# Kernel optimization log

Measured on AMD Instinct MI355X. Metric: run time of the kernel, lower is better.

## Reference

```python
import jax, jax.numpy as jnp
import numpy as np

C = 10  # cluster gap window; repo-level global constant in the original code


def _per_neuron(v, label):
    """Faithful vectorized translation of the per-(batch,neuron) Python loops.

    v:     [T] membrane potential trace
    label: scalar int target cluster count
    Returns (loss_contribution, num_cluster).
    """
    T = v.shape[0]
    t = jnp.arange(T, dtype=jnp.int32)
    spk = v >= 0.0                                   # spike positions (v >= 0)
    # exclusive prefix counts of spikes: csp[i] = #spikes in v[:i]
    csp = jnp.concatenate([jnp.zeros(1, jnp.int32), jnp.cumsum(spk.astype(jnp.int32))])
    lo = jnp.clip(t - C, 0, T)
    # a spike starts a new cluster iff no spike in the preceding C steps
    cnt_prev = csp[t] - csp[lo]
    is_start = spk & (cnt_prev == 0)
    num_cluster = jnp.sum(is_start.astype(jnp.int32))
    vmax = jnp.max(v)

    # ---- excess branch (label > num_cluster) ----
    # mask[t] = 1 iff some spike lies in [t-C, t+C]  (union of [first-C, last+C] per cluster)
    hi = jnp.clip(t + C + 1, 0, T)
    mask = (csp[hi] - csp[lo]) > 0
    full0 = jnp.all(mask)
    NEG = jnp.asarray(-1e30, v.dtype)
    m0 = jnp.max(jnp.where(mask, NEG, v))            # max over unmasked times (iter 0)
    tm = jnp.argmax(v)                               # original uses global argmax of v
    win = (t >= tm - C // 2) & (t <= tm + C // 2)
    mask2 = mask | win                               # mask after first loop iteration (fixed thereafter)
    full2 = jnp.all(mask2)
    # if mask2 full, remaining iterations pick a spike value (random in original; spikes have v>=0,
    # we use the deterministic surrogate vmax which is always a spike value when spikes exist)
    m_rest = jnp.where(full2, vmax, jnp.max(jnp.where(mask2, NEG, v)))
    label_f = label.astype(v.dtype)
    ncf = num_cluster.astype(v.dtype)
    dE = jnp.maximum(label_f - ncf, 1.0)             # safe denominator (branch-gated below)
    mean_excess = (m0 + (dE - 1.0) * m_rest) / dE
    excess_loss = jnp.where(full0, vmax, -mean_excess)

    # ---- deficit branch (label < num_cluster) ----
    BIG = T + 2 * C + 2
    lt = jax.lax.cummax(jnp.where(spk, t, -BIG))                 # nearest spike <= t
    rt = jax.lax.cummin(jnp.where(spk, t, BIG)[::-1])[::-1]      # nearest spike >= t
    in_span = (rt - lt) <= C                                     # t inside [first,last] of a cluster
    cid = jnp.cumsum(is_start.astype(jnp.int32)) - 1             # cluster id at time t
    K = T // (C + 1) + 1                                         # max possible clusters
    seg = jnp.where(in_span, cid, K)
    rec = jax.ops.segment_max(v, seg, num_segments=K + 1)[:K]    # per-cluster span max
    POS = jnp.asarray(1e30, v.dtype)
    rec = jnp.where(jnp.arange(K) < num_cluster, rec, POS)
    rec = jnp.sort(rec)                                          # ascending, real clusters first
    dD = jnp.maximum(ncf - label_f, 1.0)
    deficit_loss = jnp.sum(jnp.where(jnp.arange(K) < (num_cluster - label), rec, 0.0)) / dD

    contrib = jnp.where(label > num_cluster, excess_loss,
                        jnp.where(label < num_cluster, deficit_loss, 0.0))
    return contrib, num_cluster


def setup_inputs() -> dict:
    key = jax.random.key(0)
    k1, k2, k3 = jax.random.split(key, 3)
    B, T, N = 256, 500, 128
    vmem = jax.random.normal(k1, (B, T, N), dtype=jnp.float32)
    vlastmem = jax.random.normal(k2, (B, T, N), dtype=jnp.float32)
    labels_t = jax.random.randint(k3, (B, N), 0, 5, dtype=jnp.int32)
    return {"vmem": vmem, "vlastmem": vlastmem, "labels_t": labels_t, "ratio": 1}


def reference(vmem, vlastmem, labels_t, ratio):
    # vlastmem and ratio are unused in the original forward; kept for signature fidelity.
    vv = jnp.transpose(vmem, (0, 2, 1))  # [B, N, T]
    contrib, nclus = jax.vmap(jax.vmap(_per_neuron))(vv, labels_t)
    loss = jnp.sum(contrib)
    spike_output = nclus.astype(jnp.float32)  # [B, N] cluster counts
    return loss, spike_output
```

## Files before the change

kernel.cpp:

```cpp
#include <hip/hip_runtime.h>

namespace {
constexpr int CC    = 10;
constexpr int TT    = 500;
constexpr int NN    = 128;
constexpr int G     = 10;
constexpr int LSEG  = TT / G;
constexpr int HALO  = CC;
constexpr int NSLOT = 10;
constexpr int MAXG  = TT / (CC + 1) + 1;
}

__global__ __launch_bounds__(128, 5)
void seg_scan_kernel(const float* __restrict__ vmem, float* __restrict__ ws) {
    const int s   = blockIdx.x;
    const int b   = blockIdx.y;
    const int tid = threadIdx.x;
    const int a   = s * LSEG;
    const float* __restrict__ col = vmem + (size_t)b * TT * NN + tid;

    __shared__ float stg[5 * NN];

    float b0[10], b1[10], b2[10], b3[10] = {};
    auto load = [&](float (&d)[10], int c) {
        #pragma unroll
        for (int j = 0; j < 10; ++j) {
            int t = a + (-HALO + 10 * c + j);
            t = t < 0 ? 0 : (t > TT - 1 ? TT - 1 : t);
            d[j] = col[(size_t)t * NN];
        }
    };

    int   ls = -(1 << 20), lcount = 0, hdne = 0, tmn = 0, hasu = 0;
    float ccm = -1e30f, rmax = -1e30f, hdm = -1e30f, vmx = -1e30f, m0 = -1e30f;
    const bool firstSeg = (s == 0), lastSeg = (s == G - 1);
    #pragma unroll
    for (int i = 0; i < 5; ++i) stg[i * NN + tid] = 0.0f;

    auto scan = [&](const float (&cur)[10], const float (&prev)[10], int c) {
        #pragma unroll
        for (int j = 0; j < 10; ++j) {
            const int ofs = -HALO + 10 * c + j;
            const int t   = a + ofs;
            float v = cur[j];
            if ((ofs < 0 && firstSeg) || (ofs >= LSEG && lastSeg)) v = -1.0f;
            const bool spike = v >= 0.0f;
            if (ofs >= 0 && ofs < LSEG) {
                const float rm2 = fmaxf(rmax, v);
                if (spike) {
                    if (t - ls > CC) {
                        if (lcount > 0) stg[(lcount - 1) * NN + tid] = ccm;
                        ccm = v; ++lcount;
                    } else if (lcount == 0) { hdne = 1; hdm = fmaxf(hdm, rm2); }
                    else ccm = fmaxf(ccm, rm2);
                    rmax = -1e30f;
                } else rmax = rm2;
                if (v > vmx) { vmx = v; tmn = t; }
            }
            if (spike) ls = t;
            if (ofs >= HALO) {
                const float vu = prev[j];
                if (ls < t - 2 * CC) { hasu = 1; if (vu > m0) m0 = vu; }
            }
        }
    };

    load(b0, 0); load(b1, 1);
    load(b2, 2); scan(b0, b3, 0);
    load(b3, 3); scan(b1, b0, 1);
    load(b0, 4); scan(b2, b1, 2);
    load(b1, 5); scan(b3, b2, 3);
    load(b2, 6); scan(b0, b3, 4);
    scan(b1, b0, 5);
    scan(b2, b1, 6);

    if (lcount > 0) stg[(lcount - 1) * NN + tid] = ccm;

    float* __restrict__ wsl = ws + (size_t)(b * G + s) * NSLOT * NN + tid;
    #pragma unroll
    for (int i = 0; i < 5; ++i) wsl[i * NN] = stg[i * NN + tid];
    const int packed = lcount | (hdne << 3) | (hasu << 4) | (tmn << 5);
    wsl[5 * NN] = __int_as_float(packed);
    wsl[6 * NN] = hdm;
    wsl[7 * NN] = rmax;
    wsl[8 * NN] = vmx;
    wsl[9 * NN] = m0;
}

__global__ __launch_bounds__(64)
void merge_kernel(const float* __restrict__ vmem, const float* __restrict__ ws,
                  const int* __restrict__ labels, float* __restrict__ out) {
    const int bb = blockIdx.x, lane = threadIdx.x;
    const int b = bb >> 1, n = ((bb & 1) << 6) | lane;
    __shared__ float gl[MAXG * 64];
    __shared__ float wb[512];

    const float* __restrict__ wsb = ws + (size_t)b * G * NSLOT * NN + n;
    float f[2][10];
    auto loadSeg = [&](int slot, int s2) {
        const float* p = wsb + (size_t)s2 * NSLOT * NN;
        #pragma unroll
        for (int i = 0; i < 10; ++i) f[slot][i] = p[i * NN];
    };
    loadSeg(0, 0);

    int g = 0, g_nc = 0, g_hasu = 0, g_tm = 0;
    bool open = false; float cur = -1e30f, ptg = -1e30f;
    float g_vmax = -1e30f, g_m0 = -1e30f;
    #pragma unroll
    for (int s2 = 0; s2 < G; ++s2) {
        if (s2 + 1 < G) loadSeg((s2 + 1) & 1, s2 + 1);
        const float (&d)[10] = f[s2 & 1];
        const int pk = __float_as_int(d[5]);
        const int k = pk & 7, hne = (pk >> 3) & 1;
        g_nc += k; g_hasu |= (pk >> 4) & 1;
        if (d[8] > g_vmax) { g_vmax = d[8]; g_tm = pk >> 5; }
        if (d[9] > g_m0) g_m0 = d[9];
        if (open) {
            if (hne) { cur = fmaxf(cur, fmaxf(ptg, d[6])); ptg = d[7]; }
            if (k > 0 || !hne) { gl[g * 64 + lane] = cur; ++g; open = false; }
        }
        if (k > 0) {
            #pragma unroll
            for (int i = 0; i < 4; ++i)
                if (i < k - 1) { gl[g * 64 + lane] = d[i]; ++g; }
            float last = d[4];
            if (k == 1) last = d[0];
            else if (k == 2) last = d[1];
            else if (k == 3) last = d[2];
            else if (k == 4) last = d[3];
            cur = last; open = true; ptg = d[7];
        }
    }
    if (open) { gl[g * 64 + lane] = cur; ++g; }

    const int label = labels[b * NN + n];

    const bool need2 = (label > g_nc) && g_hasu && (label - g_nc >= 2);
    float mrest = g_vmax;
    unsigned long long bal = __ballot(need2);
    const float* colbase = vmem + (size_t)b * TT * NN;
    while (bal) {
        const int fl = __ffsll((unsigned long long)bal) - 1;
        bal &= bal - 1;
        const int   nf    = ((bb & 1) << 6) | fl;
        const int   tmf   = __shfl(g_tm, fl);
        const float vmaxf = __shfl(g_vmax, fl);
        #pragma unroll
        for (int j = 0; j < 8; ++j) {
            const int t = lane * 8 + j;
            wb[t] = (t < TT) ? colbase[(size_t)t * NN + nf] : -1.0f;
        }
        __syncthreads();
        int ls2 = -1000, lh = 0; float lm = -1e30f;
        const int u0 = lane * 8;
        for (int t2 = u0 - 10; t2 < u0 + 18; ++t2) {
            const float v = (t2 >= 0 && t2 < 512) ? wb[t2] : -1.0f;
            if (v >= 0.0f) ls2 = t2;
            const int u = t2 - 10;
            if (u >= u0 && u < u0 + 8 && u < TT) {
                if (ls2 < u - 10 && (u < tmf - CC / 2 || u > tmf + CC / 2)) {
                    lh = 1; const float vu = wb[u]; if (vu > lm) lm = vu;
                }
            }
        }
        #pragma unroll
        for (int off = 32; off > 0; off >>= 1) {
            lm = fmaxf(lm, __shfl_down(lm, off));
            lh |= __shfl_down(lh, off);
        }
        const float res = __shfl(lh ? lm : vmaxf, 0);
        if (lane == fl) mrest = res;
        __syncthreads();
    }

    float contrib = 0.0f;
    if (label > g_nc) {
        if (!g_hasu) contrib = g_vmax;
        else {
            const float dE = (float)(label - g_nc);
            contrib = -((g_m0 + (dE - 1.0f) * mrest) / dE);
        }
    } else if (label < g_nc) {
        const int kk = g_nc - label;
        float ssum = 0.0f;
        for (int i = 0; i < kk; ++i) {
            float mn = 1e30f; int mj = 0;
            for (int jj = 0; jj < g_nc; ++jj) {
                const float x = gl[jj * 64 + lane];
                if (x < mn) { mn = x; mj = jj; }
            }
            ssum += mn; gl[mj * 64 + lane] = 1e30f;
        }
        contrib = ssum / (float)kk;
    }

    out[1 + b * NN + n] = (float)g_nc;

    float w = contrib;
    #pragma unroll
    for (int off = 32; off > 0; off >>= 1) w += __shfl_down(w, off);
    if (lane == 0) atomicAdd(out, w);
}

extern "C" void kernel_launch(void* const* d_in, const int* in_sizes, int n_in,
                              void* d_out, int out_size, void* d_ws, size_t ws_size,
                              hipStream_t stream) {
    const float* vmem   = (const float*)d_in[0];
    const int*   labels = (const int*)d_in[2];
    float*       out    = (float*)d_out;
    float*       ws     = (float*)d_ws;

    const int B = in_sizes[2] / NN;

    hipMemsetAsync(out, 0, sizeof(float), stream);
    hipLaunchKernelGGL(seg_scan_kernel, dim3(G, B), dim3(NN), 0, stream, vmem, ws);
    hipLaunchKernelGGL(merge_kernel, dim3(2 * B), dim3(64), 0, stream, vmem, ws, labels, out);
}
```

Measured before the change: 164.5 us.

## Load whole segment into registers and make the scan loop branchless

Replaces the rotating 4-buffer software-pipelined load/scan with a single upfront load of all 70 rows into registers. The per-row cluster scan becomes branch-free selects, and the current cluster max is written to shared memory on every step instead of only when a cluster closes. Unused slots are zeroed at write-out. Occupancy hint drops from 5 to 4 blocks per CU to make room for the extra registers. All loads are issued early to expose memory parallelism, at the cost of higher register pressure and more LDS stores.

```diff
diff --git a/kernel.cpp b/kernel.cpp
--- a/kernel.cpp
+++ b/kernel.cpp
@@ -7,11 +7,12 @@
 constexpr int G     = 10;
 constexpr int LSEG  = TT / G;
 constexpr int HALO  = CC;
+constexpr int ROWS  = LSEG + 2 * HALO;
 constexpr int NSLOT = 10;
 constexpr int MAXG  = TT / (CC + 1) + 1;
 }
 
-__global__ __launch_bounds__(128, 5)
+__global__ __launch_bounds__(128, 4)
 void seg_scan_kernel(const float* __restrict__ vmem, float* __restrict__ ws) {
     const int s   = blockIdx.x;
     const int b   = blockIdx.y;
@@ -21,64 +22,60 @@
 
     __shared__ float stg[5 * NN];
 
-    float b0[10], b1[10], b2[10], b3[10] = {};
-    auto load = [&](float (&d)[10], int c) {
-        #pragma unroll
-        for (int j = 0; j < 10; ++j) {
-            int t = a + (-HALO + 10 * c + j);
-            t = t < 0 ? 0 : (t > TT - 1 ? TT - 1 : t);
-            d[j] = col[(size_t)t * NN];
-        }
-    };
+    float v[ROWS];
+    #pragma unroll
+    for (int r = 0; r < ROWS; ++r) {
+        int t = a - HALO + r;
+        t = t < 0 ? 0 : (t > TT - 1 ? TT - 1 : t);
+        v[r] = col[(size_t)t * NN];
+    }
+    if (s == 0) {
+        #pragma unroll
+        for (int r = 0; r < HALO; ++r) v[r] = -1.0f;
+    }
+    if (s == G - 1) {
+        #pragma unroll
+        for (int r = LSEG + HALO; r < ROWS; ++r) v[r] = -1.0f;
+    }
 
     int   ls = -(1 << 20), lcount = 0, hdne = 0, tmn = 0, hasu = 0;
     float ccm = -1e30f, rmax = -1e30f, hdm = -1e30f, vmx = -1e30f, m0 = -1e30f;
-    const bool firstSeg = (s == 0), lastSeg = (s == G - 1);
-    #pragma unroll
-    for (int i = 0; i < 5; ++i) stg[i * NN + tid] = 0.0f;
-
-    auto scan = [&](const float (&cur)[10], const float (&prev)[10], int c) {
-        #pragma unroll
-        for (int j = 0; j < 10; ++j) {
-            const int ofs = -HALO + 10 * c + j;
-            const int t   = a + ofs;
-            float v = cur[j];
-            if ((ofs < 0 && firstSeg) || (ofs >= LSEG && lastSeg)) v = -1.0f;
-            const bool spike = v >= 0.0f;
-            if (ofs >= 0 && ofs < LSEG) {
-                const float rm2 = fmaxf(rmax, v);
-                if (spike) {
-                    if (t - ls > CC) {
-                        if (lcount > 0) stg[(lcount - 1) * NN + tid] = ccm;
-                        ccm = v; ++lcount;
-                    } else if (lcount == 0) { hdne = 1; hdm = fmaxf(hdm, rm2); }
-                    else ccm = fmaxf(ccm, rm2);
-                    rmax = -1e30f;
-                } else rmax = rm2;
-                if (v > vmx) { vmx = v; tmn = t; }
-            }
-            if (spike) ls = t;
-            if (ofs >= HALO) {
-                const float vu = prev[j];
-                if (ls < t - 2 * CC) { hasu = 1; if (vu > m0) m0 = vu; }
-            }
-        }
-    };
-
-    load(b0, 0); load(b1, 1);
-    load(b2, 2); scan(b0, b3, 0);
-    load(b3, 3); scan(b1, b0, 1);
-    load(b0, 4); scan(b2, b1, 2);
-    load(b1, 5); scan(b3, b2, 3);
-    load(b2, 6); scan(b0, b3, 4);
-    scan(b1, b0, 5);
-    scan(b2, b1, 6);
-
-    if (lcount > 0) stg[(lcount - 1) * NN + tid] = ccm;
+
+    #pragma unroll
+    for (int r = 0; r < ROWS; ++r) {
+        const int ofs = r - HALO;
+        const int t   = a + ofs;
+        const float x = v[r];
+        const bool spike = x >= 0.0f;
+        if (ofs >= 0 && ofs < LSEG) {
+            const float rm2     = fmaxf(rmax, x);
+            const bool  recent  = (t - ls <= CC);
+            const bool  isStart = spike && !recent;
+            const bool  contS   = spike && recent;
+            const bool  hd      = contS && (lcount == 0);
+            hdm  = hd ? fmaxf(hdm, rm2) : hdm;
+            hdne = hd ? 1 : hdne;
+            const float folded = fmaxf(ccm, rm2);
+            ccm  = isStart ? x : ((contS && lcount > 0) ? folded : ccm);
+            lcount += isStart ? 1 : 0;
+            rmax = spike ? -1e30f : rm2;
+            if (x > vmx) { vmx = x; tmn = t; }
+            const int idx = lcount > 0 ? lcount - 1 : 0;
+            stg[idx * NN + tid] = ccm;
+        }
+        if (spike) ls = t;
+        if (r >= 2 * HALO) {
+            const float vu = v[r - HALO];
+            const bool  um = ls < t - 2 * CC;
+            hasu = um ? 1 : hasu;
+            m0   = um ? fmaxf(m0, vu) : m0;
+        }
+    }
 
     float* __restrict__ wsl = ws + (size_t)(b * G + s) * NSLOT * NN + tid;
     #pragma unroll
-    for (int i = 0; i < 5; ++i) wsl[i * NN] = stg[i * NN + tid];
+    for (int i = 0; i < 5; ++i)
+        wsl[i * NN] = (i < lcount) ? stg[i * NN + tid] : 0.0f;
     const int packed = lcount | (hdne << 3) | (hasu << 4) | (tmn << 5);
     wsl[5 * NN] = __int_as_float(packed);
     wsl[6 * NN] = hdm;
```

After: 256.2 us. 55.7% more time.

## Pack more wavefronts per block and make segment scan branch-free

Applied to the files above, without the earlier changes.

The segment scan kernel now packs ten wavefronts into a 640-thread block, with each wave covering one segment-half and using its own shared staging area. The scan body is rewritten as predicated selects, and it writes the current cluster max to shared memory on every step instead of only at cluster boundaries. The merge kernel now runs four independent wavefronts per 256-thread block with per-wave shared buffers, and replaces __syncthreads with block fences because each wave only touches its own buffers. The aim is to cut block count and launch and scheduling overhead and to reduce divergence, at the cost of extra shared stores per step and lower occupancy from the larger blocks.

```diff
diff --git a/kernel.cpp b/kernel.cpp
--- a/kernel.cpp
+++ b/kernel.cpp
@@ -11,15 +11,20 @@
 constexpr int MAXG  = TT / (CC + 1) + 1;
 }
 
-__global__ __launch_bounds__(128, 5)
+__global__ __launch_bounds__(640, 5)
 void seg_scan_kernel(const float* __restrict__ vmem, float* __restrict__ ws) {
-    const int s   = blockIdx.x;
-    const int b   = blockIdx.y;
-    const int tid = threadIdx.x;
-    const int a   = s * LSEG;
-    const float* __restrict__ col = vmem + (size_t)b * TT * NN + tid;
-
-    __shared__ float stg[5 * NN];
+    const int z    = blockIdx.x;
+    const int b    = blockIdx.y;
+    const int tid  = threadIdx.x;
+    const int ww   = tid >> 6;
+    const int lane = tid & 63;
+    const int s    = z * 5 + (ww >> 1);
+    const int half = ww & 1;
+    const int a    = s * LSEG;
+    const float* __restrict__ col = vmem + (size_t)b * TT * NN + half * 64 + lane;
+
+    __shared__ float stg[10][5 * 64];
+    float* sw = stg[ww];
 
     float b0[10], b1[10], b2[10], b3[10] = {};
     auto load = [&](float (&d)[10], int c) {
@@ -34,33 +39,37 @@
     int   ls = -(1 << 20), lcount = 0, hdne = 0, tmn = 0, hasu = 0;
     float ccm = -1e30f, rmax = -1e30f, hdm = -1e30f, vmx = -1e30f, m0 = -1e30f;
     const bool firstSeg = (s == 0), lastSeg = (s == G - 1);
-    #pragma unroll
-    for (int i = 0; i < 5; ++i) stg[i * NN + tid] = 0.0f;
 
     auto scan = [&](const float (&cur)[10], const float (&prev)[10], int c) {
         #pragma unroll
         for (int j = 0; j < 10; ++j) {
             const int ofs = -HALO + 10 * c + j;
             const int t   = a + ofs;
-            float v = cur[j];
-            if ((ofs < 0 && firstSeg) || (ofs >= LSEG && lastSeg)) v = -1.0f;
-            const bool spike = v >= 0.0f;
+            float x = cur[j];
+            if ((ofs < 0 && firstSeg) || (ofs >= LSEG && lastSeg)) x = -1.0f;
+            const bool spike = x >= 0.0f;
             if (ofs >= 0 && ofs < LSEG) {
-                const float rm2 = fmaxf(rmax, v);
-                if (spike) {
-                    if (t - ls > CC) {
-                        if (lcount > 0) stg[(lcount - 1) * NN + tid] = ccm;
-                        ccm = v; ++lcount;
-                    } else if (lcount == 0) { hdne = 1; hdm = fmaxf(hdm, rm2); }
-                    else ccm = fmaxf(ccm, rm2);
-                    rmax = -1e30f;
-                } else rmax = rm2;
-                if (v > vmx) { vmx = v; tmn = t; }
+                const float rm2     = fmaxf(rmax, x);
+                const bool  recent  = (t - ls <= CC);
+                const bool  isStart = spike && !recent;
+                const bool  contS   = spike && recent;
+                const bool  hd      = contS && (lcount == 0);
+                hdm  = hd ? fmaxf(hdm, rm2) : hdm;
+                hdne = hd ? 1 : hdne;
+                const float folded = fmaxf(ccm, rm2);
+                ccm  = isStart ? x : ((contS && lcount > 0) ? folded : ccm);
+                lcount += isStart ? 1 : 0;
+                rmax = spike ? -1e30f : rm2;
+                if (x > vmx) { vmx = x; tmn = t; }
+                const int idx = lcount > 0 ? lcount - 1 : 0;
+                sw[idx * 64 + lane] = ccm;
             }
             if (spike) ls = t;
             if (ofs >= HALO) {
                 const float vu = prev[j];
-                if (ls < t - 2 * CC) { hasu = 1; if (vu > m0) m0 = vu; }
+                const bool  um = ls < t - 2 * CC;
+                hasu = um ? 1 : hasu;
+                m0   = um ? fmaxf(m0, vu) : m0;
             }
         }
     };
@@ -74,11 +83,12 @@
     scan(b1, b0, 5);
     scan(b2, b1, 6);
 
-    if (lcount > 0) stg[(lcount - 1) * NN + tid] = ccm;
-
-    float* __restrict__ wsl = ws + (size_t)(b * G + s) * NSLOT * NN + tid;
+    if (lcount > 0) sw[(lcount - 1) * 64 + lane] = ccm;
+
+    float* __restrict__ wsl = ws + (size_t)(b * G + s) * NSLOT * NN + half * 64 + lane;
     #pragma unroll
-    for (int i = 0; i < 5; ++i) wsl[i * NN] = stg[i * NN + tid];
+    for (int i = 0; i < 5; ++i)
+        wsl[i * NN] = (i < lcount) ? sw[i * 64 + lane] : 0.0f;
     const int packed = lcount | (hdne << 3) | (hasu << 4) | (tmn << 5);
     wsl[5 * NN] = __int_as_float(packed);
     wsl[6 * NN] = hdm;
@@ -87,13 +97,16 @@
     wsl[9 * NN] = m0;
 }
 
-__global__ __launch_bounds__(64)
+__global__ __launch_bounds__(256)
 void merge_kernel(const float* __restrict__ vmem, const float* __restrict__ ws,
                   const int* __restrict__ labels, float* __restrict__ out) {
-    const int bb = blockIdx.x, lane = threadIdx.x;
+    const int tid = threadIdx.x, ww = tid >> 6, lane = tid & 63;
+    const int bb = blockIdx.x * 4 + ww;
     const int b = bb >> 1, n = ((bb & 1) << 6) | lane;
-    __shared__ float gl[MAXG * 64];
-    __shared__ float wb[512];
+    __shared__ float gl[4][MAXG * 64];
+    __shared__ float wb4[4][512];
+    float* glw = gl[ww];
+    float* wb  = wb4[ww];
 
     const float* __restrict__ wsb = ws + (size_t)b * G * NSLOT * NN + n;
     float f[2][10];
@@ -118,12 +131,12 @@
         if (d[9] > g_m0) g_m0 = d[9];
         if (open) {
             if (hne) { cur = fmaxf(cur, fmaxf(ptg, d[6])); ptg = d[7]; }
-            if (k > 0 || !hne) { gl[g * 64 + lane] = cur; ++g; open = false; }
+            if (k > 0 || !hne) { glw[g * 64 + lane] = cur; ++g; open = false; }
         }
         if (k > 0) {
             #pragma unroll
             for (int i = 0; i < 4; ++i)
-                if (i < k - 1) { gl[g * 64 + lane] = d[i]; ++g; }
+                if (i < k - 1) { glw[g * 64 + lane] = d[i]; ++g; }
             float last = d[4];
             if (k == 1) last = d[0];
             else if (k == 2) last = d[1];
@@ -132,7 +145,7 @@
             cur = last; open = true; ptg = d[7];
         }
     }
-    if (open) { gl[g * 64 + lane] = cur; ++g; }
+    if (open) { glw[g * 64 + lane] = cur; ++g; }
 
     const int label = labels[b * NN + n];
 
@@ -151,7 +164,7 @@
             const int t = lane * 8 + j;
             wb[t] = (t < TT) ? colbase[(size_t)t * NN + nf] : -1.0f;
         }
-        __syncthreads();
+        __threadfence_block();
         int ls2 = -1000, lh = 0; float lm = -1e30f;
         const int u0 = lane * 8;
         for (int t2 = u0 - 10; t2 < u0 + 18; ++t2) {
@@ -171,7 +184,7 @@
         }
         const float res = __shfl(lh ? lm : vmaxf, 0);
         if (lane == fl) mrest = res;
-        __syncthreads();
+        __threadfence_block();
     }
 
     float contrib = 0.0f;
@@ -187,10 +200,10 @@
         for (int i = 0; i < kk; ++i) {
             float mn = 1e30f; int mj = 0;
             for (int jj = 0; jj < g_nc; ++jj) {
-                const float x = gl[jj * 64 + lane];
+                const float x = glw[jj * 64 + lane];
                 if (x < mn) { mn = x; mj = jj; }
             }
-            ssum += mn; gl[mj * 64 + lane] = 1e30f;
+            ssum += mn; glw[mj * 64 + lane] = 1e30f;
         }
         contrib = ssum / (float)kk;
     }
@@ -214,6 +227,6 @@
     const int B = in_sizes[2] / NN;
 
     hipMemsetAsync(out, 0, sizeof(float), stream);
-    hipLaunchKernelGGL(seg_scan_kernel, dim3(G, B), dim3(NN), 0, stream, vmem, ws);
-    hipLaunchKernelGGL(merge_kernel, dim3(2 * B), dim3(64), 0, stream, vmem, ws, labels, out);
-}
+    hipLaunchKernelGGL(seg_scan_kernel, dim3(2, B), dim3(640), 0, stream, vmem, ws);
+    hipLaunchKernelGGL(merge_kernel, dim3(B / 2), dim3(256), 0, stream, vmem, ws, labels, out);
+}
```

New measurement: 296.7 us. 1.8x slower.
